# Optimization experiments

Hardware: AMD Instinct MI355X
Metric: run time of the kernel (lower is better)

Reference implementation:

```python
import jax, jax.numpy as jnp
from jax import lax
import numpy as np

HEADS, SAMPLES = 4, 8
B, C, D, H, W = 1, 64, 16, 64, 64
HD = C // HEADS  # head_dim = 16
BN_EPS = 1e-5


def conv3d(x, w, b=None, pad=0):
    out = lax.conv_general_dilated(
        x, w, (1, 1, 1), [(pad, pad)] * 3,
        dimension_numbers=("NCDHW", "OIDHW", "NCDHW"))
    if b is not None:
        out = out + b[None, :, None, None, None]
    return out


def trilinear_sample(vol, grid):
    # vol: [Dv,Hv,Wv,Cc]; grid: [...,3] with torch grid_sample semantics:
    # grid[...,0] -> x (W axis), grid[...,1] -> y (H axis), grid[...,2] -> z (D axis)
    # align_corners=True, padding_mode='border'. Returns [..., Cc].
    Dv, Hv, Wv, _ = vol.shape
    ix = (grid[..., 0] + 1.0) * 0.5 * (Wv - 1)
    iy = (grid[..., 1] + 1.0) * 0.5 * (Hv - 1)
    iz = (grid[..., 2] + 1.0) * 0.5 * (Dv - 1)
    x0 = jnp.floor(ix); y0 = jnp.floor(iy); z0 = jnp.floor(iz)
    wx = (ix - x0)[..., None]; wy = (iy - y0)[..., None]; wz = (iz - z0)[..., None]
    x0i = jnp.clip(x0.astype(jnp.int32), 0, Wv - 1); x1i = jnp.clip(x0i + 1, 0, Wv - 1)
    y0i = jnp.clip(y0.astype(jnp.int32), 0, Hv - 1); y1i = jnp.clip(y0i + 1, 0, Hv - 1)
    z0i = jnp.clip(z0.astype(jnp.int32), 0, Dv - 1); z1i = jnp.clip(z0i + 1, 0, Dv - 1)
    g = lambda z, y, x: vol[z, y, x]
    out = (g(z0i, y0i, x0i) * (1 - wz) * (1 - wy) * (1 - wx)
           + g(z0i, y0i, x1i) * (1 - wz) * (1 - wy) * wx
           + g(z0i, y1i, x0i) * (1 - wz) * wy * (1 - wx)
           + g(z0i, y1i, x1i) * (1 - wz) * wy * wx
           + g(z1i, y0i, x0i) * wz * (1 - wy) * (1 - wx)
           + g(z1i, y0i, x1i) * wz * (1 - wy) * wx
           + g(z1i, y1i, x0i) * wz * wy * (1 - wx)
           + g(z1i, y1i, x1i) * wz * wy * wx)
    return out


def t_deform(feat_prev, feat_curr, p):
    b, c, d, h, w = feat_curr.shape
    kv = conv3d(feat_prev, p["kv_w"], p["kv_b"])          # [B,2C,D,H,W]
    q = conv3d(feat_curr, p["q_w"], p["q_b"])              # [B,C,D,H,W]
    # offset branch: conv3x3 -> GELU(exact) -> conv3x3(no bias) -> tanh
    o = conv3d(feat_curr, p["off1_w"], p["off1_b"], pad=1)
    o = jax.nn.gelu(o, approximate=False)
    o = jnp.tanh(conv3d(o, p["off2_w"], None, pad=1))      # [B,M*S*3,D,H,W]
    off = o.reshape(b, HEADS, SAMPLES, 3, d, h, w).transpose(0, 1, 4, 5, 6, 2, 3)  # [B,M,D,H,W,S,3]
    zz, yy, xx = jnp.meshgrid(jnp.linspace(-1, 1, d), jnp.linspace(-1, 1, h),
                              jnp.linspace(-1, 1, w), indexing="ij")
    base = jnp.stack((zz, yy, xx), axis=-1).astype(feat_curr.dtype)  # [D,H,W,3]
    scale = jnp.array([d, h, w], dtype=feat_curr.dtype)
    grid = base[None, None, :, :, :, None, :] + off / scale
    grid = jnp.clip(grid, -1.0, 1.0)
    grid = grid.transpose(0, 1, 5, 2, 3, 4, 6).reshape(b * HEADS, SAMPLES, d, h, w, 3)
    # channels-last per (batch,head) volume; avoids torch's explicit repeat over samples
    vols = kv.reshape(b, HEADS, 2 * HD, d, h, w).transpose(0, 1, 3, 4, 5, 2)
    vols = vols.reshape(b * HEADS, d, h, w, 2 * HD)
    sampled = jax.vmap(trilinear_sample)(vols, grid)        # [B*M,S,D,H,W,2*HD]
    sampled = sampled.reshape(b, HEADS, SAMPLES, d, h, w, 2 * HD)
    key, value = sampled[..., :HD], sampled[..., HD:]
    qh = q.reshape(b, HEADS, HD, d, h, w) * (HD ** -0.5)
    attn = jnp.einsum("bmcdhw,bmsdhwc->bmsdhw", qh, key)
    attn = jax.nn.softmax(attn, axis=2)
    fused = jnp.einsum("bmsdhw,bmsdhwc->bmcdhw", attn, value).reshape(b, c, d, h, w)
    out = conv3d(fused, p["out_w"], p["out_b"])
    # BatchNorm3d (eval: running stats) + ReLU
    inv = lax.rsqrt(p["bn_var"] + BN_EPS)
    out = (out - p["bn_mean"][None, :, None, None, None]) * (inv * p["bn_gamma"])[None, :, None, None, None] \
          + p["bn_beta"][None, :, None, None, None]
    return jax.nn.relu(out)


def setup_inputs() -> dict:
    key = jax.random.key(0)
    ks = jax.random.split(key, 16)
    r = lambda k, shp, s=0.05: (jax.random.normal(k, shp, dtype=jnp.float32) * s)
    return {
        "mid_feat": jax.random.normal(ks[0], (B, C, D, H, W), dtype=jnp.float32),
        "occ_feat": jax.random.normal(ks[1], (B, C, D, H, W), dtype=jnp.float32),
        "prev_feat": jax.random.normal(ks[2], (B, C, D, H, W), dtype=jnp.float32),
        "off1_w": r(ks[3], (C, C, 3, 3, 3)), "off1_b": r(ks[4], (C,)),
        "off2_w": r(ks[5], (HEADS * SAMPLES * 3, C, 3, 3, 3)),
        "kv_w": r(ks[6], (2 * C, C, 1, 1, 1)), "kv_b": r(ks[7], (2 * C,)),
        "q_w": r(ks[8], (C, C, 1, 1, 1)), "q_b": r(ks[9], (C,)),
        "out_w": r(ks[10], (C, C, 1, 1, 1)), "out_b": r(ks[11], (C,)),
        "bn_gamma": jnp.ones((C,), jnp.float32), "bn_beta": jnp.zeros((C,), jnp.float32),
        "bn_mean": jnp.zeros((C,), jnp.float32), "bn_var": jnp.ones((C,), jnp.float32),
    }


def reference(mid_feat, occ_feat, prev_feat, off1_w, off1_b, off2_w, kv_w, kv_b,
              q_w, q_b, out_w, out_b, bn_gamma, bn_beta, bn_mean, bn_var):
    p = dict(off1_w=off1_w, off1_b=off1_b, off2_w=off2_w, kv_w=kv_w, kv_b=kv_b,
             q_w=q_w, q_b=q_b, out_w=out_w, out_b=out_b, bn_gamma=bn_gamma,
             bn_beta=bn_beta, bn_mean=bn_mean, bn_var=bn_var)
    d1 = t_deform(mid_feat, occ_feat, p)
    d2 = t_deform(mid_feat, prev_feat, p)
    return jnp.concatenate([mid_feat, d1, d2], axis=1)  # [B,3C,D,H,W]
```

## Files before the change

kernel.cpp:

```cpp
#include <hip/hip_runtime.h>
#include <math.h>

#define DD 16
#define HH 64
#define WW 64
#define VV (DD*HH*WW)
#define CC 64
#define NHEADS 4
#define NSAMP 8
#define HDIM 16

typedef unsigned int uint;
typedef unsigned short ushort;
typedef __attribute__((ext_vector_type(8))) short bf16x8;
typedef __attribute__((ext_vector_type(4))) float f32x4;

__device__ __forceinline__ float clampf(float v, float lo, float hi){ return fminf(fmaxf(v, lo), hi); }
__device__ __forceinline__ int imin(int a, int b){ return a < b ? a : b; }

__device__ __forceinline__ ushort f2bf(float f){
  uint u = __float_as_uint(f);
  uint r = (u + 0x7fffu + ((u>>16)&1u)) >> 16;
  return (ushort)r;
}
__device__ __forceinline__ uint packbf2(float a, float b){
  return (uint)f2bf(a) | ((uint)f2bf(b) << 16);
}
__device__ __forceinline__ float bflo(uint u){ return __uint_as_float(u << 16); }
__device__ __forceinline__ float bfhi(uint u){ return __uint_as_float(u & 0xffff0000u); }
__device__ __forceinline__ float bf2f(ushort u){ return __uint_as_float((uint)u << 16); }

__device__ __forceinline__ float fast_tanh(float x){
  float e = __expf(2.f*x);
  return 1.f - 2.f/(e + 1.f);
}

__global__ __launch_bounds__(256) void pack_in(const float* __restrict__ a,
                                               const float* __restrict__ b,
                                               uint* __restrict__ o){
  int idx = blockIdx.x*256 + threadIdx.x;
  int v4 = (idx & (VV/4 - 1)) * 4;
  int rest = idx >> 14;
  int cp = rest & 31;
  int call = rest >> 5;
  const float* x = call ? b : a;
  float4 f0 = *reinterpret_cast<const float4*>(x + (size_t)(2*cp)*VV + v4);
  float4 f1 = *reinterpret_cast<const float4*>(x + (size_t)(2*cp+1)*VV + v4);
  uint4 pk;
  pk.x = packbf2(f0.x, f1.x);
  pk.y = packbf2(f0.y, f1.y);
  pk.z = packbf2(f0.z, f1.z);
  pk.w = packbf2(f0.w, f1.w);
  *reinterpret_cast<uint4*>(o + (size_t)(call*32+cp)*VV + v4) = pk;
}

__global__ void repack_wmfma(const float* __restrict__ w, uint* __restrict__ o, int MG){
  int U = blockIdx.x*256 + threadIdx.x;
  int total = 54*MG*256;
  if (U >= total) return;
  int j2 = U & 3;
  int m  = (U>>2) & 15;
  int q  = (U>>6) & 3;
  int rest = U >> 8;
  int g = rest % MG;
  int s = rest / MG;
  int tap = s >> 1, h = s & 1;
  int co = g*16 + m;
  int ci = h*32 + q*8 + j2*2;
  int base = co*1728 + ci*27 + tap;
  o[U] = packbf2(w[base], w[base + 27]);
}
__global__ void repack_w1mfma(const float* __restrict__ w, uint* __restrict__ o, int MT){
  int U = blockIdx.x*256 + threadIdx.x;
  int total = 2*MT*256;
  if (U >= total) return;
  int j2 = U & 3;
  int lane = (U>>2) & 63;
  int frag = U >> 8;
  int mt = frag % MT;
  int ks = frag / MT;
  int q = lane >> 4, m = lane & 15;
  int co = mt*16 + m;
  int ci = ks*32 + q*8 + j2*2;
  o[U] = packbf2(w[co*CC + ci], w[co*CC + ci + 1]);
}

template<int CO, int EPI>
__global__ __launch_bounds__(256) void conv1_mfma(
    const void* __restrict__ xa, const void* __restrict__ xb,
    const uint* __restrict__ wA, const float* __restrict__ bias,
    void* __restrict__ outp)
{
  constexpr int MT = CO/16;
  constexpr int MW = MT/4;
  __shared__ ushort xt[64*72];
  int tid = threadIdx.x;
  int lane = tid & 63;
  int g = __builtin_amdgcn_readfirstlane(tid >> 6);
  int q = lane >> 4, n = lane & 15;
  int call = blockIdx.x >> 10;
  int v0 = (blockIdx.x & 1023) * 64;
  if constexpr (EPI == 0){
    const float* x = call ? (const float*)xb : (const float*)xa;
    for (int it = tid; it < 64*32; it += 256){
      int vox = it & 63; int cp = it >> 6;
      float a = x[(size_t)(2*cp)*VV + v0 + vox];
      float b = x[(size_t)(2*cp+1)*VV + v0 + vox];
      *reinterpret_cast<uint*>(&xt[vox*72 + 2*cp]) = packbf2(a,b);
    }
  } else {
    const uint* xp = (const uint*)xa + (size_t)call*32*VV;
    for (int it = tid; it < 64*32; it += 256){
      int vox = it & 63; int cp = it >> 6;
      *reinterpret_cast<uint*>(&xt[vox*72 + 2*cp]) = xp[(size_t)cp*VV + v0 + vox];
    }
  }
  __syncthreads();
  f32x4 acc[MW][4];
  #pragma unroll
  for (int mw=0;mw<MW;mw++)
    #pragma unroll
    for (int nt=0;nt<4;nt++){ acc[mw][nt].x=0.f; acc[mw][nt].y=0.f; acc[mw][nt].z=0.f; acc[mw][nt].w=0.f; }
  const char* ldsb = reinterpret_cast<const char*>(xt);
  const char* wac  = reinterpret_cast<const char*>(wA);
  #pragma unroll
  for (int ks=0; ks<2; ks++){
    bf16x8 bfr[4];
    #pragma unroll
    for (int nt=0; nt<4; nt++)
      bfr[nt] = *reinterpret_cast<const bf16x8*>(ldsb + ((nt*16+n)*144 + q*16 + ks*64));
    #pragma unroll
    for (int mw=0; mw<MW; mw++){
      int mt = g*MW + mw;
      bf16x8 af = *reinterpret_cast<const bf16x8*>(wac + (size_t)((ks*MT + mt)*64 + lane)*16);
      #pragma unroll
      for (int nt=0; nt<4; nt++)
        acc[mw][nt] = __builtin_amdgcn_mfma_f32_16x16x32_bf16(af, bfr[nt], acc[mw][nt], 0, 0, 0);
    }
  }
  if constexpr (EPI == 0){
    #pragma unroll
    for (int mw=0; mw<MW; mw++){
      int mt = g*MW + mw;
      int cob = mt*16 + q*4;
      #pragma unroll
      for (int nt=0; nt<4; nt++){
        int v = v0 + nt*16 + n;
        float r0 = acc[mw][nt].x + bias[cob+0];
        float r1 = acc[mw][nt].y + bias[cob+1];
        float r2 = acc[mw][nt].z + bias[cob+2];
        float r3 = acc[mw][nt].w + bias[cob+3];
        int z = v >> 12, y = (v >> 6) & 63, xx = v & 63;
        int head = cob >> 5;
        uint* vols = (uint*)outp;
        uint2 pk; pk.x = packbf2(r0,r1); pk.y = packbf2(r2,r3);
        *reinterpret_cast<uint2*>(vols + ((size_t)head*VV + (size_t)(y*WW+xx)*DD + z)*16 + ((cob&31)>>1)) = pk;
      }
    }
  } else {
    __syncthreads();
    ushort* xr = xt;
    int cob = g*16 + q*4;
    #pragma unroll
    for (int nt=0; nt<4; nt++){
      int vox = nt*16 + n;
      uint2 pk;
      pk.x = packbf2((acc[0][nt].x + bias[cob+0])*0.25f, (acc[0][nt].y + bias[cob+1])*0.25f);
      pk.y = packbf2((acc[0][nt].z + bias[cob+2])*0.25f, (acc[0][nt].w + bias[cob+3])*0.25f);
      *reinterpret_cast<uint2*>(&xr[vox*64 + cob]) = pk;
    }
    __syncthreads();
    char* ob = (char*)((ushort*)outp + (size_t)call*CC*VV) + (size_t)v0*128;
    const char* lb = reinterpret_cast<const char*>(xr);
    #pragma unroll
    for (int k=0; k<2; k++){
      int idx = tid + k*256;
      *reinterpret_cast<uint4*>(ob + idx*16) = *reinterpret_cast<const uint4*>(lb + idx*16);
    }
  }
}

template<int CO, int OUTPK>
__global__ __launch_bounds__(256) void conv3_mfma(
    const uint* __restrict__ xpk,
    const uint* __restrict__ wA, const float* __restrict__ bias,
    void* __restrict__ outp)
{
  constexpr int MG = CO/16;
  constexpr int MROW = CO/32;
  __shared__ ushort xh[400*40];
  int tid = threadIdx.x;
  int lane = tid & 63;
  int w = __builtin_amdgcn_readfirstlane(tid >> 6);
  int q = lane >> 4, n = lane & 15;
  int bid = blockIdx.x;
  int xcd = bid & 7, islot = bid >> 3;
  int call = islot >> 6;
  int z0 = xcd*2;
  int rem = islot & 63;
  int by = (rem >> 3) << 3, bx = (rem & 7) << 3;

  const uint* xinp = xpk + (size_t)call*32*VV;

  int mbase = (w & 1) * MROW;
  int nh = w >> 1;
  int lo[4];
  #pragma unroll
  for (int nt=0;nt<4;nt++){
    int vl = nt*16 + n;
    lo[nt] = ((nh*100 + (vl>>3)*10 + (vl&7)))*80 + q*16;
  }
  f32x4 acc[MROW][4];
  #pragma unroll
  for (int mr=0;mr<MROW;mr++)
    #pragma unroll
    for (int nt=0;nt<4;nt++){ acc[mr][nt].x=0.f; acc[mr][nt].y=0.f; acc[mr][nt].z=0.f; acc[mr][nt].w=0.f; }

  const char* ldsb = reinterpret_cast<const char*>(xh);
  const char* wac  = reinterpret_cast<const char*>(wA);

  uint pa[13], pb[13];
  auto load_half = [&](int h){
    #pragma unroll
    for (int k=0;k<13;k++){
      int it = tid + k*256;
      if (it < 3200){
        int cg = it/400; int pos = it - cg*400;
        int dz = pos/100; int rr = pos - dz*100; int dy = rr/10; int dxx = rr - dy*10;
        int gz = z0 + dz - 1, gy = by + dy - 1, gx = bx + dxx - 1;
        uint a = 0u, b = 0u;
        if (gz>=0 && gz<DD && gy>=0 && gy<HH && gx>=0 && gx<WW){
          size_t gv = (size_t)((gz*HH+gy)*WW + gx);
          int cp0 = h*16 + cg*2;
          a = xinp[(size_t)cp0*VV + gv];
          b = xinp[(size_t)(cp0+1)*VV + gv];
        }
        pa[k] = a; pb[k] = b;
      }
    }
  };
  auto write_half = [&](){
    #pragma unroll
    for (int k=0;k<13;k++){
      int it = tid + k*256;
      if (it < 3200){
        int cg = it/400; int pos = it - cg*400;
        uint2 pk; pk.x = pa[k]; pk.y = pb[k];
        *reinterpret_cast<uint2*>(&xh[pos*40 + cg*4]) = pk;
      }
    }
  };
  auto compute_half = [&](int h){
    #pragma unroll 3
    for (int tap=0; tap<27; tap++){
      int dz = tap/9; int r9 = tap - dz*9; int dy = r9/3; int dxx = r9 - dy*3;
      int stepOff = (dz*100 + dy*10 + dxx)*80;
      int s = tap*2 + h;
      bf16x8 af[MROW];
      #pragma unroll
      for (int mr=0;mr<MROW;mr++)
        af[mr] = *reinterpret_cast<const bf16x8*>(wac + (size_t)((s*MG + mbase+mr)*64 + lane)*16);
      bf16x8 bf[4];
      #pragma unroll
      for (int nt=0;nt<4;nt++)
        bf[nt] = *reinterpret_cast<const bf16x8*>(ldsb + (lo[nt] + stepOff));
      #pragma unroll
      for (int mr=0;mr<MROW;mr++)
        #pragma unroll
        for (int nt=0;nt<4;nt++)
          acc[mr][nt] = __builtin_amdgcn_mfma_f32_16x16x32_bf16(af[mr], bf[nt], acc[mr][nt], 0, 0, 0);
    }
  };

  load_half(0);
  write_half();
  __syncthreads();
  load_half(1);
  compute_half(0);
  __syncthreads();
  write_half();
  __syncthreads();
  compute_half(1);

  if (OUTPK == 1){
    #pragma unroll
    for (int mr=0; mr<MROW; mr++){
      int cob = (mbase+mr)*16 + q*4;
      #pragma unroll
      for (int nt=0; nt<4; nt++){
        int vl = nt*16 + n;
        int vy = by + (vl>>3), vx = bx + (vl&7);
        size_t gv = (size_t)(((z0+nh)*HH + vy)*WW + vx);
        float r0 = acc[mr][nt].x + bias[cob+0];
        float r1 = acc[mr][nt].y + bias[cob+1];
        float r2 = acc[mr][nt].z + bias[cob+2];
        float r3 = acc[mr][nt].w + bias[cob+3];
        r0 = 0.5f*r0*(1.f + erff(r0*0.70710678118654752f));
        r1 = 0.5f*r1*(1.f + erff(r1*0.70710678118654752f));
        r2 = 0.5f*r2*(1.f + erff(r2*0.70710678118654752f));
        r3 = 0.5f*r3*(1.f + erff(r3*0.70710678118654752f));
        uint* dst = (uint*)outp + (size_t)call*32*VV;
        dst[(size_t)(cob>>1)*VV + gv]     = packbf2(r0,r1);
        dst[(size_t)((cob>>1)+1)*VV + gv] = packbf2(r2,r3);
      }
    }
  } else {
    __syncthreads();
    ushort* xr = xh;
    #pragma unroll
    for (int mr=0; mr<MROW; mr++){
      int cob = (mbase+mr)*16 + q*4;
      #pragma unroll
      for (int nt=0; nt<4; nt++){
        int row = nh*64 + nt*16 + n;
        uint2 pk;
        pk.x = packbf2(fast_tanh(acc[mr][nt].x), fast_tanh(acc[mr][nt].y));
        pk.y = packbf2(fast_tanh(acc[mr][nt].z), fast_tanh(acc[mr][nt].w));
        *reinterpret_cast<uint2*>(&xr[row*96 + cob]) = pk;
      }
    }
    __syncthreads();
    ushort* dst = (ushort*)outp + (size_t)call*96*VV;
    const char* lb = reinterpret_cast<const char*>(xr);
    #pragma unroll
    for (int k=0; k<6; k++){
      int idx = tid + k*256;
      int chunk = idx/96;
      int off = idx - chunk*96;
      int zi = chunk>>3, y8 = chunk&7;
      size_t gb = (size_t)(((z0+zi)*HH + by + y8)*WW + bx)*192 + (size_t)off*16;
      *reinterpret_cast<uint4*>((char*)dst + gb) = *reinterpret_cast<const uint4*>(lb + idx*16);
    }
  }
}

struct Geom { int x0,x1,y0,y1,z0,z1; float wx,wy,wz; };
__device__ __forceinline__ Geom make_geom(float zb, float yb, float xb,
                                          float o0, float o1, float o2){
  float g0 = clampf(zb + o0*(1.f/16.f), -1.f, 1.f);
  float g1 = clampf(yb + o1*(1.f/64.f), -1.f, 1.f);
  float g2 = clampf(xb + o2*(1.f/64.f), -1.f, 1.f);
  float ix = (g0+1.f)*0.5f*63.f;
  float iy = (g1+1.f)*0.5f*63.f;
  float iz = (g2+1.f)*0.5f*15.f;
  float fx=floorf(ix), fy=floorf(iy), fz=floorf(iz);
  Geom g;
  g.wx = ix-fx; g.wy = iy-fy; g.wz = iz-fz;
  g.x0 = (int)fx; g.x1 = imin(g.x0+1, WW-1);
  g.y0 = (int)fy; g.y1 = imin(g.y0+1, HH-1);
  g.z0 = (int)fz; g.z1 = imin(g.z0+1, DD-1);
  return g;
}

__global__ __launch_bounds__(256) void sample_attn_kernel(
    const ushort* __restrict__ qbuf, const ushort* __restrict__ offbuf,
    const uint* __restrict__ vols, const uint* __restrict__ woA,
    const float* __restrict__ outb, const float* __restrict__ bng,
    const float* __restrict__ bnb, const float* __restrict__ bnm,
    const float* __restrict__ bnv, float* __restrict__ dout)
{
  __shared__ ushort fsb[16*72];
  int t = threadIdx.x;
  int lane = t & 63;
  int m = __builtin_amdgcn_readfirstlane(t >> 6);
  int slot = lane >> 2;
  int r = lane & 3;
  int bid = blockIdx.x;
  int xcd = bid & 7, islot = bid >> 3;
  int call = islot >> 9;
  int z = xcd*2 + ((islot >> 8) & 1);
  int rem = islot & 255;
  int y = rem >> 2;
  int x0 = (rem & 3) << 4;
  int x = x0 + slot;
  int vbase = (z*HH + y)*WW + x0;
  int v = vbase + slot;

  const ushort* qb = qbuf   + (size_t)call*CC*VV;
  const ushort* ob = offbuf + (size_t)call*96*VV;

  uint4 qu = *reinterpret_cast<const uint4*>(qb + (size_t)v*64 + m*16 + (r&1)*8);
  float qf[8];
  qf[0]=bflo(qu.x); qf[1]=bfhi(qu.x); qf[2]=bflo(qu.y); qf[3]=bfhi(qu.y);
  qf[4]=bflo(qu.z); qf[5]=bfhi(qu.z); qf[6]=bflo(qu.w); qf[7]=bfhi(qu.w);

  uint ou[12];
  {
    const uint4* op4 = reinterpret_cast<const uint4*>(ob + (size_t)v*96 + m*24);
    uint4 a = op4[0], b4 = op4[1], c4 = op4[2];
    ou[0]=a.x;  ou[1]=a.y;  ou[2]=a.z;  ou[3]=a.w;
    ou[4]=b4.x; ou[5]=b4.y; ou[6]=b4.z; ou[7]=b4.w;
    ou[8]=c4.x; ou[9]=c4.y; ou[10]=c4.z; ou[11]=c4.w;
  }

  float zbf = -1.f + (float)z*(2.f/15.f);
  float ybf = -1.f + (float)y*(2.f/63.f);
  float xbf = -1.f + (float)x*(2.f/63.f);

  const char* volb = reinterpret_cast<const char*>(vols) + (size_t)m*VV*64;
  float roleK = (r < 2) ? 1.f : 0.f;
  float lrun = 0.f;
  float fused[8];
  #pragma unroll
  for (int c=0;c<8;c++) fused[c]=0.f;

  #pragma unroll
  for (int s=0;s<NSAMP;s++){
    int i0 = 3*s, i1 = 3*s+1, i2 = 3*s+2;
    float o0 = (i0&1) ? bfhi(ou[i0>>1]) : bflo(ou[i0>>1]);
    float o1 = (i1&1) ? bfhi(ou[i1>>1]) : bflo(ou[i1>>1]);
    float o2 = (i2&1) ? bfhi(ou[i2>>1]) : bflo(ou[i2>>1]);
    Geom g = make_geom(zbf,ybf,xbf,o0,o1,o2);
    int tz0 = g.z0*64 + r*16;
    int tz1 = g.z1*64 + r*16;
    float wx1 = g.wx, wx0 = 1.f-g.wx;
    float wy1 = g.wy, wy0 = 1.f-g.wy;
    float wz1 = g.wz, wz0 = 1.f-g.wz;
    float acc[8];
    #pragma unroll
    for (int c=0;c<8;c++) acc[c]=0.f;
    #pragma unroll
    for (int ky=0;ky<2;ky++)
    #pragma unroll
    for (int kx=0;kx<2;kx++){
      int cy = ky? g.y1:g.y0, cx = kx? g.x1:g.x0;
      float wyx = (ky? wy1:wy0)*(kx? wx1:wx0);
      float a0 = wyx*wz0, a1 = wyx*wz1;
      uint wzp;
      asm("v_cvt_pk_bf16_f32 %0, %1, %2" : "=v"(wzp) : "v"(a0), "v"(a1));
      int tb = ((cy<<6) + cx) << 10;
      const char* p = volb + tb;
      uint4 u0 = *reinterpret_cast<const uint4*>(p + tz0);
      uint4 u1 = *reinterpret_cast<const uint4*>(p + tz1);
      uint plo, phi;
      plo = __builtin_amdgcn_perm(u1.x, u0.x, 0x05040100u);
      phi = __builtin_amdgcn_perm(u1.x, u0.x, 0x07060302u);
      asm("v_dot2_f32_bf16 %0, %1, %2, %0" : "+v"(acc[0]) : "v"(plo), "v"(wzp));
      asm("v_dot2_f32_bf16 %0, %1, %2, %0" : "+v"(acc[1]) : "v"(phi), "v"(wzp));
      plo = __builtin_amdgcn_perm(u1.y, u0.y, 0x05040100u);
      phi = __builtin_amdgcn_perm(u1.y, u0.y, 0x07060302u);
      asm("v_dot2_f32_bf16 %0, %1, %2, %0" : "+v"(acc[2]) : "v"(plo), "v"(wzp));
      asm("v_dot2_f32_bf16 %0, %1, %2, %0" : "+v"(acc[3]) : "v"(phi), "v"(wzp));
      plo = __builtin_amdgcn_perm(u1.z, u0.z, 0x05040100u);
      phi = __builtin_amdgcn_perm(u1.z, u0.z, 0x07060302u);
      asm("v_dot2_f32_bf16 %0, %1, %2, %0" : "+v"(acc[4]) : "v"(plo), "v"(wzp));
      asm("v_dot2_f32_bf16 %0, %1, %2, %0" : "+v"(acc[5]) : "v"(phi), "v"(wzp));
      plo = __builtin_amdgcn_perm(u1.w, u0.w, 0x05040100u);
      phi = __builtin_amdgcn_perm(u1.w, u0.w, 0x07060302u);
      asm("v_dot2_f32_bf16 %0, %1, %2, %0" : "+v"(acc[6]) : "v"(plo), "v"(wzp));
      asm("v_dot2_f32_bf16 %0, %1, %2, %0" : "+v"(acc[7]) : "v"(phi), "v"(wzp));
    }
    float h = qf[0]*acc[0]+qf[1]*acc[1]+qf[2]*acc[2]+qf[3]*acc[3]
            + qf[4]*acc[4]+qf[5]*acc[5]+qf[6]*acc[6]+qf[7]*acc[7];
    h *= roleK;
    h += __shfl_xor(h, 1);
    h += __shfl_xor(h, 2);
    float e = __expf(h);
    lrun += e;
    #pragma unroll
    for (int c=0;c<8;c++) fused[c] += e*acc[c];
  }
  float isum = 1.f/lrun;
  if (r >= 2){
    uint4 pk;
    pk.x = packbf2(fused[0]*isum, fused[1]*isum);
    pk.y = packbf2(fused[2]*isum, fused[3]*isum);
    pk.z = packbf2(fused[4]*isum, fused[5]*isum);
    pk.w = packbf2(fused[6]*isum, fused[7]*isum);
    *reinterpret_cast<uint4*>(&fsb[slot*72 + m*16 + (r&1)*8]) = pk;
  }
  __syncthreads();

  int qq = lane >> 4, n = lane & 15;
  f32x4 acco;
  acco.x=0.f; acco.y=0.f; acco.z=0.f; acco.w=0.f;
  const char* ldsb = reinterpret_cast<const char*>(fsb);
  const char* wac  = reinterpret_cast<const char*>(woA);
  #pragma unroll
  for (int ks=0; ks<2; ks++){
    bf16x8 af = *reinterpret_cast<const bf16x8*>(wac + (size_t)((ks*4 + m)*64 + lane)*16);
    bf16x8 bfv = *reinterpret_cast<const bf16x8*>(ldsb + (n*144 + qq*16 + ks*64));
    acco = __builtin_amdgcn_mfma_f32_16x16x32_bf16(af, bfv, acco, 0, 0, 0);
  }
  int choff = 64 + call*64;
  #pragma unroll
  for (int rr=0; rr<4; rr++){
    int co = m*16 + qq*4 + rr;
    float inv = rsqrtf(bnv[co] + 1e-5f) * bng[co];
    float val = (acco[rr] + outb[co] - bnm[co]) * inv + bnb[co];
    val = fmaxf(val, 0.f);
    dout[(size_t)(choff+co)*VV + vbase + n] = val;
  }
}

extern "C" void kernel_launch(void* const* d_in, const int* in_sizes, int n_in,
                              void* d_out, int out_size, void* d_ws, size_t ws_size,
                              hipStream_t stream){
  (void)in_sizes; (void)n_in; (void)out_size; (void)ws_size;
  const float* mid  = (const float*)d_in[0];
  const float* occ  = (const float*)d_in[1];
  const float* prev = (const float*)d_in[2];
  const float* off1w= (const float*)d_in[3];
  const float* off1b= (const float*)d_in[4];
  const float* off2w= (const float*)d_in[5];
  const float* kvw  = (const float*)d_in[6];
  const float* kvb  = (const float*)d_in[7];
  const float* qw   = (const float*)d_in[8];
  const float* qb   = (const float*)d_in[9];
  const float* outw = (const float*)d_in[10];
  const float* outb = (const float*)d_in[11];
  const float* bng  = (const float*)d_in[12];
  const float* bnb  = (const float*)d_in[13];
  const float* bnm  = (const float*)d_in[14];
  const float* bnv  = (const float*)d_in[15];
  float* out = (float*)d_out;

  uint*   vols  = (uint*)d_ws;
  ushort* qbuf  = (ushort*)(vols + (size_t)4*VV*16);
  uint*   o1pk  = (uint*)(qbuf + (size_t)2*CC*VV);
  ushort* offb  = (ushort*)(o1pk + (size_t)2*32*VV);
  uint*   wA1   = (uint*)(offb + (size_t)2*96*VV);
  uint*   wA2   = wA1 + 55296;
  uint*   wo    = wA2 + 82944;
  uint*   wkv   = wo  + 2048;
  uint*   wq    = wkv + 4096;
  uint*   o0pk  = wq  + 2048;

  pack_in<<<4096, 256, 0, stream>>>(occ, prev, o0pk);
  repack_wmfma<<<(55296+255)/256, 256, 0, stream>>>(off1w, wA1, 4);
  repack_wmfma<<<(82944+255)/256, 256, 0, stream>>>(off2w, wA2, 6);
  repack_w1mfma<<<8, 256, 0, stream>>>(outw, wo, 4);
  repack_w1mfma<<<16, 256, 0, stream>>>(kvw, wkv, 8);
  repack_w1mfma<<<8, 256, 0, stream>>>(qw, wq, 4);
  conv1_mfma<128,0><<<1024, 256, 0, stream>>>(mid, mid, wkv, kvb, (void*)vols);
  hipMemcpyAsync(out, mid, (size_t)CC*VV*sizeof(float), hipMemcpyDeviceToDevice, stream);
  conv1_mfma<64,1><<<2048, 256, 0, stream>>>(o0pk, nullptr, wq, qb, (void*)qbuf);
  conv3_mfma<64,1><<<1024, 256, 0, stream>>>(o0pk, wA1, off1b, (void*)o1pk);
  conv3_mfma<96,0><<<1024, 256, 0, stream>>>(o1pk, wA2, off1b, (void*)offb);
  sample_attn_kernel<<<8192, 256, 0, stream>>>(qbuf, offb, vols, wo,
      outb, bng, bnb, bnm, bnv, out);
}
```

Measured before the change: 337.7 us.

## Merge prep kernels, fold mid copy into kv conv, enlarge conv3 z-tile

Folds the input bf16 packing and all weight repacks into one prep launch, and changes the packed activation layout to 4-channel (uint2) groups. The hipMemcpy of mid into the output is folded into the kv 1x1 conv, which already reads mid. The 3x3x3 conv blocks now cover 4 z-slices instead of 2, with 8 N-tiles per wave, halving the grid and cutting halo reload overhead. The cost is more accumulator registers and larger LDS per block, which may reduce occupancy.

Result: faster. 327.6 us (-3.0%).

```diff
diff --git a/kernel.cpp b/kernel.cpp
--- a/kernel.cpp
+++ b/kernel.cpp
@@ -35,29 +35,8 @@
   return 1.f - 2.f/(e + 1.f);
 }
 
-__global__ __launch_bounds__(256) void pack_in(const float* __restrict__ a,
-                                               const float* __restrict__ b,
-                                               uint* __restrict__ o){
-  int idx = blockIdx.x*256 + threadIdx.x;
-  int v4 = (idx & (VV/4 - 1)) * 4;
-  int rest = idx >> 14;
-  int cp = rest & 31;
-  int call = rest >> 5;
-  const float* x = call ? b : a;
-  float4 f0 = *reinterpret_cast<const float4*>(x + (size_t)(2*cp)*VV + v4);
-  float4 f1 = *reinterpret_cast<const float4*>(x + (size_t)(2*cp+1)*VV + v4);
-  uint4 pk;
-  pk.x = packbf2(f0.x, f1.x);
-  pk.y = packbf2(f0.y, f1.y);
-  pk.z = packbf2(f0.z, f1.z);
-  pk.w = packbf2(f0.w, f1.w);
-  *reinterpret_cast<uint4*>(o + (size_t)(call*32+cp)*VV + v4) = pk;
-}
-
-__global__ void repack_wmfma(const float* __restrict__ w, uint* __restrict__ o, int MG){
-  int U = blockIdx.x*256 + threadIdx.x;
-  int total = 54*MG*256;
-  if (U >= total) return;
+__device__ __forceinline__ void repack_wmfma_body(const float* __restrict__ w,
+                                                  uint* __restrict__ o, int MG, int U){
   int j2 = U & 3;
   int m  = (U>>2) & 15;
   int q  = (U>>6) & 3;
@@ -70,10 +49,8 @@
   int base = co*1728 + ci*27 + tap;
   o[U] = packbf2(w[base], w[base + 27]);
 }
-__global__ void repack_w1mfma(const float* __restrict__ w, uint* __restrict__ o, int MT){
-  int U = blockIdx.x*256 + threadIdx.x;
-  int total = 2*MT*256;
-  if (U >= total) return;
+__device__ __forceinline__ void repack_w1_body(const float* __restrict__ w,
+                                               uint* __restrict__ o, int MT, int U){
   int j2 = U & 3;
   int lane = (U>>2) & 63;
   int frag = U >> 8;
@@ -85,11 +62,49 @@
   o[U] = packbf2(w[co*CC + ci], w[co*CC + ci + 1]);
 }
 
+__global__ __launch_bounds__(256) void prep(
+    const float* __restrict__ occ, const float* __restrict__ prev,
+    uint* __restrict__ o0pk,
+    const float* __restrict__ off1w, uint* __restrict__ wA1,
+    const float* __restrict__ off2w, uint* __restrict__ wA2,
+    const float* __restrict__ outw, uint* __restrict__ wo,
+    const float* __restrict__ kvw,  uint* __restrict__ wkv,
+    const float* __restrict__ qw,   uint* __restrict__ wq)
+{
+  int b = blockIdx.x, tid = threadIdx.x;
+  if (b < 2048){
+    int idx = b*256 + tid;
+    int v4 = (idx & (VV/4 - 1)) * 4;
+    int rest = idx >> 14;
+    int cq = rest & 15;
+    int call = rest >> 4;
+    const float* x = call ? prev : occ;
+    const float* p0 = x + (size_t)(cq*4)*VV + v4;
+    float4 f0 = *reinterpret_cast<const float4*>(p0);
+    float4 f1 = *reinterpret_cast<const float4*>(p0 + VV);
+    float4 f2 = *reinterpret_cast<const float4*>(p0 + 2*VV);
+    float4 f3 = *reinterpret_cast<const float4*>(p0 + 3*VV);
+    uint* ob = o0pk + ((size_t)(call*16 + cq)*VV + v4)*2;
+    uint4 w0, w1;
+    w0.x = packbf2(f0.x, f1.x); w0.y = packbf2(f2.x, f3.x);
+    w0.z = packbf2(f0.y, f1.y); w0.w = packbf2(f2.y, f3.y);
+    w1.x = packbf2(f0.z, f1.z); w1.y = packbf2(f2.z, f3.z);
+    w1.z = packbf2(f0.w, f1.w); w1.w = packbf2(f2.w, f3.w);
+    *reinterpret_cast<uint4*>(ob)     = w0;
+    *reinterpret_cast<uint4*>(ob + 4) = w1;
+  }
+  else if (b < 2264){ repack_wmfma_body(off1w, wA1, 4, (b-2048)*256 + tid); }
+  else if (b < 2588){ repack_wmfma_body(off2w, wA2, 6, (b-2264)*256 + tid); }
+  else if (b < 2596){ repack_w1_body(outw, wo, 4, (b-2588)*256 + tid); }
+  else if (b < 2612){ repack_w1_body(kvw, wkv, 8, (b-2596)*256 + tid); }
+  else              { repack_w1_body(qw,  wq, 4, (b-2612)*256 + tid); }
+}
+
 template<int CO, int EPI>
 __global__ __launch_bounds__(256) void conv1_mfma(
-    const void* __restrict__ xa, const void* __restrict__ xb,
+    const float* __restrict__ xf, const uint* __restrict__ xq,
     const uint* __restrict__ wA, const float* __restrict__ bias,
-    void* __restrict__ outp)
+    void* __restrict__ outp, float* __restrict__ mcopy)
 {
   constexpr int MT = CO/16;
   constexpr int MW = MT/4;
@@ -101,18 +116,19 @@
   int call = blockIdx.x >> 10;
   int v0 = (blockIdx.x & 1023) * 64;
   if constexpr (EPI == 0){
-    const float* x = call ? (const float*)xb : (const float*)xa;
     for (int it = tid; it < 64*32; it += 256){
       int vox = it & 63; int cp = it >> 6;
-      float a = x[(size_t)(2*cp)*VV + v0 + vox];
-      float b = x[(size_t)(2*cp+1)*VV + v0 + vox];
+      float a = xf[(size_t)(2*cp)*VV + v0 + vox];
+      float b = xf[(size_t)(2*cp+1)*VV + v0 + vox];
+      mcopy[(size_t)(2*cp)*VV + v0 + vox] = a;
+      mcopy[(size_t)(2*cp+1)*VV + v0 + vox] = b;
       *reinterpret_cast<uint*>(&xt[vox*72 + 2*cp]) = packbf2(a,b);
     }
   } else {
-    const uint* xp = (const uint*)xa + (size_t)call*32*VV;
-    for (int it = tid; it < 64*32; it += 256){
-      int vox = it & 63; int cp = it >> 6;
-      *reinterpret_cast<uint*>(&xt[vox*72 + 2*cp]) = xp[(size_t)cp*VV + v0 + vox];
+    const uint2* xp = reinterpret_cast<const uint2*>(xq) + (size_t)call*16*VV;
+    for (int it = tid; it < 64*16; it += 256){
+      int vox = it & 63; int cq = it >> 6;
+      *reinterpret_cast<uint2*>(&xt[vox*72 + cq*4]) = xp[(size_t)cq*VV + v0 + vox];
     }
   }
   __syncthreads();
@@ -188,70 +204,65 @@
 {
   constexpr int MG = CO/16;
   constexpr int MROW = CO/32;
-  __shared__ ushort xh[400*40];
+  __shared__ ushort xh[24576];
   int tid = threadIdx.x;
   int lane = tid & 63;
   int w = __builtin_amdgcn_readfirstlane(tid >> 6);
   int q = lane >> 4, n = lane & 15;
   int bid = blockIdx.x;
   int xcd = bid & 7, islot = bid >> 3;
-  int call = islot >> 6;
-  int z0 = xcd*2;
-  int rem = islot & 63;
-  int by = (rem >> 3) << 3, bx = (rem & 7) << 3;
-
-  const uint* xinp = xpk + (size_t)call*32*VV;
+  int call = xcd >> 2;
+  int z0 = (xcd & 3) * 4;
+  int by = (islot >> 3) << 3, bx = (islot & 7) << 3;
+
+  const uint2* xinp = reinterpret_cast<const uint2*>(xpk) + (size_t)call*16*VV;
 
   int mbase = (w & 1) * MROW;
-  int nh = w >> 1;
-  int lo[4];
-  #pragma unroll
-  for (int nt=0;nt<4;nt++){
-    int vl = nt*16 + n;
-    lo[nt] = ((nh*100 + (vl>>3)*10 + (vl&7)))*80 + q*16;
-  }
-  f32x4 acc[MROW][4];
+  int nzh = (w >> 1) * 2;
+  int lo[8];
+  #pragma unroll
+  for (int nt=0;nt<8;nt++){
+    int zi = nzh + (nt>>2);
+    int vl = (nt&3)*16 + n;
+    lo[nt] = (zi*100 + (vl>>3)*10 + (vl&7))*80 + q*16;
+  }
+  f32x4 acc[MROW][8];
   #pragma unroll
   for (int mr=0;mr<MROW;mr++)
     #pragma unroll
-    for (int nt=0;nt<4;nt++){ acc[mr][nt].x=0.f; acc[mr][nt].y=0.f; acc[mr][nt].z=0.f; acc[mr][nt].w=0.f; }
+    for (int nt=0;nt<8;nt++){ acc[mr][nt].x=0.f; acc[mr][nt].y=0.f; acc[mr][nt].z=0.f; acc[mr][nt].w=0.f; }
 
   const char* ldsb = reinterpret_cast<const char*>(xh);
   const char* wac  = reinterpret_cast<const char*>(wA);
 
-  uint pa[13], pb[13];
+  uint2 pq[19];
   auto load_half = [&](int h){
     #pragma unroll
-    for (int k=0;k<13;k++){
+    for (int k=0;k<19;k++){
       int it = tid + k*256;
-      if (it < 3200){
-        int cg = it/400; int pos = it - cg*400;
+      if (it < 4800){
+        int cg = it/600; int pos = it - cg*600;
         int dz = pos/100; int rr = pos - dz*100; int dy = rr/10; int dxx = rr - dy*10;
         int gz = z0 + dz - 1, gy = by + dy - 1, gx = bx + dxx - 1;
-        uint a = 0u, b = 0u;
-        if (gz>=0 && gz<DD && gy>=0 && gy<HH && gx>=0 && gx<WW){
-          size_t gv = (size_t)((gz*HH+gy)*WW + gx);
-          int cp0 = h*16 + cg*2;
-          a = xinp[(size_t)cp0*VV + gv];
-          b = xinp[(size_t)(cp0+1)*VV + gv];
-        }
-        pa[k] = a; pb[k] = b;
+        uint2 v; v.x = 0u; v.y = 0u;
+        if (gz>=0 && gz<DD && gy>=0 && gy<HH && gx>=0 && gx<WW)
+          v = xinp[(size_t)(h*8+cg)*VV + (size_t)((gz*HH+gy)*WW + gx)];
+        pq[k] = v;
       }
     }
   };
   auto write_half = [&](){
     #pragma unroll
-    for (int k=0;k<13;k++){
+    for (int k=0;k<19;k++){
       int it = tid + k*256;
-      if (it < 3200){
-        int cg = it/400; int pos = it - cg*400;
-        uint2 pk; pk.x = pa[k]; pk.y = pb[k];
-        *reinterpret_cast<uint2*>(&xh[pos*40 + cg*4]) = pk;
+      if (it < 4800){
+        int cg = it/600; int pos = it - cg*600;
+        *reinterpret_cast<uint2*>(&xh[pos*40 + cg*4]) = pq[k];
       }
     }
   };
   auto compute_half = [&](int h){
-    #pragma unroll 3
+    #pragma unroll 2
     for (int tap=0; tap<27; tap++){
       int dz = tap/9; int r9 = tap - dz*9; int dy = r9/3; int dxx = r9 - dy*3;
       int stepOff = (dz*100 + dy*10 + dxx)*80;
@@ -260,14 +271,14 @@
       #pragma unroll
       for (int mr=0;mr<MROW;mr++)
         af[mr] = *reinterpret_cast<const bf16x8*>(wac + (size_t)((s*MG + mbase+mr)*64 + lane)*16);
-      bf16x8 bf[4];
-      #pragma unroll
-      for (int nt=0;nt<4;nt++)
+      bf16x8 bf[8];
+      #pragma unroll
+      for (int nt=0;nt<8;nt++)
         bf[nt] = *reinterpret_cast<const bf16x8*>(ldsb + (lo[nt] + stepOff));
       #pragma unroll
       for (int mr=0;mr<MROW;mr++)
         #pragma unroll
-        for (int nt=0;nt<4;nt++)
+        for (int nt=0;nt<8;nt++)
           acc[mr][nt] = __builtin_amdgcn_mfma_f32_16x16x32_bf16(af[mr], bf[nt], acc[mr][nt], 0, 0, 0);
     }
   };
@@ -287,10 +298,11 @@
     for (int mr=0; mr<MROW; mr++){
       int cob = (mbase+mr)*16 + q*4;
       #pragma unroll
-      for (int nt=0; nt<4; nt++){
-        int vl = nt*16 + n;
+      for (int nt=0; nt<8; nt++){
+        int zi = nzh + (nt>>2);
+        int vl = (nt&3)*16 + n;
         int vy = by + (vl>>3), vx = bx + (vl&7);
-        size_t gv = (size_t)(((z0+nh)*HH + vy)*WW + vx);
+        size_t gv = (size_t)(((z0+zi)*HH + vy)*WW + vx);
         float r0 = acc[mr][nt].x + bias[cob+0];
         float r1 = acc[mr][nt].y + bias[cob+1];
         float r2 = acc[mr][nt].z + bias[cob+2];
@@ -299,9 +311,9 @@
         r1 = 0.5f*r1*(1.f + erff(r1*0.70710678118654752f));
         r2 = 0.5f*r2*(1.f + erff(r2*0.70710678118654752f));
         r3 = 0.5f*r3*(1.f + erff(r3*0.70710678118654752f));
-        uint* dst = (uint*)outp + (size_t)call*32*VV;
-        dst[(size_t)(cob>>1)*VV + gv]     = packbf2(r0,r1);
-        dst[(size_t)((cob>>1)+1)*VV + gv] = packbf2(r2,r3);
+        uint2 pk; pk.x = packbf2(r0,r1); pk.y = packbf2(r2,r3);
+        uint* dst = (uint*)outp;
+        *reinterpret_cast<uint2*>(dst + ((size_t)(call*16 + (cob>>2))*VV + gv)*2) = pk;
       }
     }
   } else {
@@ -311,8 +323,8 @@
     for (int mr=0; mr<MROW; mr++){
       int cob = (mbase+mr)*16 + q*4;
       #pragma unroll
-      for (int nt=0; nt<4; nt++){
-        int row = nh*64 + nt*16 + n;
+      for (int nt=0; nt<8; nt++){
+        int row = (nzh + (nt>>2))*64 + (nt&3)*16 + n;
         uint2 pk;
         pk.x = packbf2(fast_tanh(acc[mr][nt].x), fast_tanh(acc[mr][nt].y));
         pk.y = packbf2(fast_tanh(acc[mr][nt].z), fast_tanh(acc[mr][nt].w));
@@ -323,7 +335,7 @@
     ushort* dst = (ushort*)outp + (size_t)call*96*VV;
     const char* lb = reinterpret_cast<const char*>(xr);
     #pragma unroll
-    for (int k=0; k<6; k++){
+    for (int k=0; k<12; k++){
       int idx = tid + k*256;
       int chunk = idx/96;
       int off = idx - chunk*96;
@@ -526,17 +538,12 @@
   uint*   wq    = wkv + 4096;
   uint*   o0pk  = wq  + 2048;
 
-  pack_in<<<4096, 256, 0, stream>>>(occ, prev, o0pk);
-  repack_wmfma<<<(55296+255)/256, 256, 0, stream>>>(off1w, wA1, 4);
-  repack_wmfma<<<(82944+255)/256, 256, 0, stream>>>(off2w, wA2, 6);
-  repack_w1mfma<<<8, 256, 0, stream>>>(outw, wo, 4);
-  repack_w1mfma<<<16, 256, 0, stream>>>(kvw, wkv, 8);
-  repack_w1mfma<<<8, 256, 0, stream>>>(qw, wq, 4);
-  conv1_mfma<128,0><<<1024, 256, 0, stream>>>(mid, mid, wkv, kvb, (void*)vols);
-  hipMemcpyAsync(out, mid, (size_t)CC*VV*sizeof(float), hipMemcpyDeviceToDevice, stream);
-  conv1_mfma<64,1><<<2048, 256, 0, stream>>>(o0pk, nullptr, wq, qb, (void*)qbuf);
-  conv3_mfma<64,1><<<1024, 256, 0, stream>>>(o0pk, wA1, off1b, (void*)o1pk);
-  conv3_mfma<96,0><<<1024, 256, 0, stream>>>(o1pk, wA2, off1b, (void*)offb);
+  prep<<<2620, 256, 0, stream>>>(occ, prev, o0pk, off1w, wA1, off2w, wA2,
+                                 outw, wo, kvw, wkv, qw, wq);
+  conv1_mfma<128,0><<<1024, 256, 0, stream>>>(mid, nullptr, wkv, kvb, (void*)vols, out);
+  conv1_mfma<64,1><<<2048, 256, 0, stream>>>(nullptr, o0pk, wq, qb, (void*)qbuf, nullptr);
+  conv3_mfma<64,1><<<512, 256, 0, stream>>>(o0pk, wA1, off1b, (void*)o1pk);
+  conv3_mfma<96,0><<<512, 256, 0, stream>>>(o1pk, wA2, off1b, (void*)offb);
   sample_attn_kernel<<<8192, 256, 0, stream>>>(qbuf, offb, vols, wo,
       outb, bng, bnb, bnm, bnv, out);
 }
```
